# Performance work log

Measured on AMD Instinct MI355X. Metric: run time of the kernel, lower is better.

Reference implementation:

```python
import jax, jax.numpy as jnp
import numpy as np

B, S, E = 1, 2048, 4096
H, D = 32, 128  # num_heads, head_dim


def setup_inputs() -> dict:
    key = jax.random.key(0)
    k1, k2, k3 = jax.random.split(key, 3)
    hidden_states = jax.random.normal(k1, (B, S, E), dtype=jnp.float32)
    # real RoPE tables (half-rotation / llama-style), base 10000
    inv_freq = 1.0 / (10000.0 ** (np.arange(0, D, 2, dtype=np.float32) / D))  # [D/2]
    pos = np.arange(S, dtype=np.float32)
    freqs = np.outer(pos, inv_freq)                      # [S, D/2]
    emb = np.concatenate([freqs, freqs], axis=-1)        # [S, D]
    cos = jnp.asarray(np.cos(emb), dtype=jnp.float32)
    sin = jnp.asarray(np.sin(emb), dtype=jnp.float32)
    w_pack = jax.random.normal(k2, (3 * E, E), dtype=jnp.float32) * (E ** -0.5)
    w_o = jax.random.normal(k3, (E, E), dtype=jnp.float32) * (E ** -0.5)
    return {"hidden_states": hidden_states, "cos": cos, "sin": sin,
            "w_pack": w_pack, "w_o": w_o}


def _rotate_half(x):
    x1, x2 = jnp.split(x, 2, axis=-1)
    return jnp.concatenate([-x2, x1], axis=-1)


def reference(hidden_states, cos, sin, w_pack, w_o):
    # fused QKV projection (W_pack, no bias)
    qkv = jnp.einsum('bse,fe->bsf', hidden_states, w_pack)      # [B,S,3E]
    q, k, v = jnp.split(qkv, 3, axis=-1)
    q = q.reshape(B, S, H, D)
    k = k.reshape(B, S, H, D)
    v = v.reshape(B, S, H, D)
    # RoPE (7B path; is_13b=False)
    c = cos[None, :, None, :]
    s = sin[None, :, None, :]
    q = q * c + _rotate_half(q) * s
    k = k * c + _rotate_half(k) * s
    # causal attention (prefill, empty past KV cache)
    scale = 1.0 / jnp.sqrt(jnp.asarray(D, dtype=q.dtype))
    scores = jnp.einsum('bqhd,bkhd->bhqk', q, k) * scale        # [B,H,S,S]
    causal = jnp.tril(jnp.ones((S, S), dtype=bool))
    scores = jnp.where(causal[None, None], scores, jnp.asarray(-1e30, scores.dtype))
    probs = jax.nn.softmax(scores, axis=-1)
    attn = jnp.einsum('bhqk,bkhd->bqhd', probs, v)              # [B,S,H,D]
    attn = attn.reshape(B, S, H * D)
    # output projection
    return jnp.einsum('bsf,ef->bse', attn, w_o)
```

## Files before the change

kernel.cpp:

```cpp
#include <hip/hip_runtime.h>

typedef unsigned short u16;
typedef unsigned int   u32;
typedef __attribute__((ext_vector_type(8))) short short8;
typedef __attribute__((ext_vector_type(4))) float f32x4;

__device__ __forceinline__ float b2f(u16 u) {
  union { float f; u32 i; } v; v.i = ((u32)u) << 16; return v.f;
}
__device__ __forceinline__ u16 f2b(float f) {
  union { float f; u32 i; } v; v.f = f;
  u32 r = v.i + 0x7fffu + ((v.i >> 16) & 1u);
  return (u16)(r >> 16);
}

__device__ __forceinline__ void gload_lds16(const void* g, void* l) {
  __builtin_amdgcn_global_load_lds(
      (const __attribute__((address_space(1))) void*)g,
      (__attribute__((address_space(3))) void*)l, 16, 0, 0);
}

template <int N> __device__ __forceinline__ void wait_vmcnt() {
  if constexpr (N == 0)      asm volatile("s_waitcnt vmcnt(0)" ::: "memory");
  else if constexpr (N == 2) asm volatile("s_waitcnt vmcnt(2)" ::: "memory");
  else if constexpr (N == 3) asm volatile("s_waitcnt vmcnt(3)" ::: "memory");
  else if constexpr (N == 4) asm volatile("s_waitcnt vmcnt(4)" ::: "memory");
  else if constexpr (N == 6) asm volatile("s_waitcnt vmcnt(6)" ::: "memory");
  else static_assert(N < 0, "unsupported vmcnt literal");
}

__device__ __forceinline__ ushort4 cvt4(float4 v) {
  ushort4 o;
  o.x = f2b(v.x); o.y = f2b(v.y); o.z = f2b(v.z); o.w = f2b(v.w);
  return o;
}

__global__ __launch_bounds__(256) void cvt_hp(const float* __restrict__ hs,
                                              const float* __restrict__ wp,
                                              u16* __restrict__ h_bf,
                                              u16* __restrict__ wp_bf) {
  const long H4 = 2097152, W4 = 12582912;
  for (long i = (long)blockIdx.x * 256 + threadIdx.x; i < H4 + W4;
       i += (long)gridDim.x * 256) {
    if (i < H4)
      ((ushort4*)h_bf)[i] = cvt4(((const float4*)hs)[i]);
    else
      ((ushort4*)wp_bf)[i - H4] = cvt4(((const float4*)wp)[i - H4]);
  }
}

__global__ __launch_bounds__(256) void cvt_bf16(const float* __restrict__ in,
                                                u16* __restrict__ out, int n4) {
  for (long i = (long)blockIdx.x * 256 + threadIdx.x; i < n4; i += (long)gridDim.x * 256)
    ((ushort4*)out)[i] = cvt4(((const float4*)in)[i]);
}

__device__ __forceinline__ short8 frag_ld64(const u16* base, int rbase, int kk,
                                            int fr, int fq) {
  const int r = rbase + fr;
  return *(const short8*)(base + r * 64 + ((((kk << 2) + fq) ^ (r & 7)) << 3));
}

__global__ __launch_bounds__(512, 2) void gemm8p(const u16* __restrict__ A,
                                                 const u16* __restrict__ B,
                                                 u16* __restrict__ Cq,
                                                 u16* __restrict__ VT,
                                                 int M, int N, int K) {
  constexpr int AE = 16384;
  constexpr int BUFSZ = AE + 12288;
  __shared__ u16 lds[2 * BUFSZ];
  const int tid = threadIdx.x;
  const int wid = tid >> 6, lane = tid & 63;
  const int fr = lane & 15, fq = lane >> 4;
  const int mA = (wid >> 2) * 128;
  const int nB = (wid & 3) * 48;

  const int nty = M >> 8;
  const int qx = gridDim.x >> 3;
  const int wg = (blockIdx.x & 7) * qx + (blockIdx.x >> 3);
  const int by = wg % nty, bx = wg / nty;
  const long row0 = (long)by * 256, col0 = (long)bx * 192;

  const int rr8 = tid >> 3;
  const int jl = (tid & 7) ^ (rr8 & 7);
  const u16* gA = A + (row0 + rr8) * (long)K + jl * 8;
  const u16* gB = B + (col0 + rr8) * (long)K + jl * 8;

  f32x4 acc[8][3];
#pragma unroll
  for (int m = 0; m < 8; ++m)
#pragma unroll
    for (int n = 0; n < 3; ++n) acc[m][n] = f32x4{0.f, 0.f, 0.f, 0.f};

  const int NT = K >> 6;

  auto stageA = [&](int i, int t) {
    gload_lds16(gA + (long)(i * 64) * K + (long)t * 64,
                lds + (t & 1) * BUFSZ + (i * 512 + tid) * 8);
  };
  auto stageB = [&](int i, int t) {
    gload_lds16(gB + (long)(i * 64) * K + (long)t * 64,
                lds + (t & 1) * BUFSZ + AE + (i * 512 + tid) * 8);
  };

#pragma unroll
  for (int i = 0; i < 4; ++i) stageA(i, 0);
#pragma unroll
  for (int i = 0; i < 3; ++i) stageB(i, 0);
#pragma unroll
  for (int i = 0; i < 3; ++i) stageB(i, 1);
  wait_vmcnt<3>();
  __builtin_amdgcn_s_barrier();

  for (int t = 0; t < NT; ++t) {
    const u16* SA = lds + (t & 1) * BUFSZ;
    const u16* SB = SA + AE;
    short8 a0[4], a1[4], b0[3], b1[3];

#pragma unroll
    for (int m = 0; m < 4; ++m) a0[m] = frag_ld64(SA, mA + m * 16, 0, fr, fq);
#pragma unroll
    for (int n = 0; n < 3; ++n) b0[n] = frag_ld64(SB, nB + n * 16, 0, fr, fq);
#pragma unroll
    for (int n = 0; n < 3; ++n) b1[n] = frag_ld64(SB, nB + n * 16, 1, fr, fq);
    if (t + 1 < NT) { stageA(0, t + 1); stageA(1, t + 1); }
    __builtin_amdgcn_s_setprio(1);
#pragma unroll
    for (int m = 0; m < 4; ++m)
#pragma unroll
      for (int n = 0; n < 3; ++n)
        acc[m][n] = __builtin_amdgcn_mfma_f32_16x16x32_bf16(a0[m], b0[n], acc[m][n], 0, 0, 0);
    __builtin_amdgcn_s_setprio(0);
    asm volatile("s_waitcnt lgkmcnt(0)" ::: "memory");
    __builtin_amdgcn_s_barrier();

#pragma unroll
    for (int m = 0; m < 4; ++m) a1[m] = frag_ld64(SA, mA + 64 + m * 16, 0, fr, fq);
    if (t + 1 < NT) { stageA(2, t + 1); stageA(3, t + 1); }
    __builtin_amdgcn_s_setprio(1);
#pragma unroll
    for (int m = 0; m < 4; ++m)
#pragma unroll
      for (int n = 0; n < 3; ++n)
        acc[4 + m][n] = __builtin_amdgcn_mfma_f32_16x16x32_bf16(a1[m], b0[n], acc[4 + m][n], 0, 0, 0);
    __builtin_amdgcn_s_setprio(0);
    __builtin_amdgcn_s_barrier();

#pragma unroll
    for (int m = 0; m < 4; ++m) a0[m] = frag_ld64(SA, mA + m * 16, 1, fr, fq);
    if (t + 2 < NT) { stageB(0, t + 2); stageB(1, t + 2); }
    __builtin_amdgcn_s_setprio(1);
#pragma unroll
    for (int m = 0; m < 4; ++m)
#pragma unroll
      for (int n = 0; n < 3; ++n)
        acc[m][n] = __builtin_amdgcn_mfma_f32_16x16x32_bf16(a0[m], b1[n], acc[m][n], 0, 0, 0);
    __builtin_amdgcn_s_setprio(0);
    __builtin_amdgcn_s_barrier();

#pragma unroll
    for (int m = 0; m < 4; ++m) a1[m] = frag_ld64(SA, mA + 64 + m * 16, 1, fr, fq);
    if (t + 2 < NT) stageB(2, t + 2);
    __builtin_amdgcn_s_setprio(1);
#pragma unroll
    for (int m = 0; m < 4; ++m)
#pragma unroll
      for (int n = 0; n < 3; ++n)
        acc[4 + m][n] = __builtin_amdgcn_mfma_f32_16x16x32_bf16(a1[m], b1[n], acc[4 + m][n], 0, 0, 0);
    __builtin_amdgcn_s_setprio(0);
    if (t + 2 < NT) wait_vmcnt<3>();
    else            wait_vmcnt<0>();
    __builtin_amdgcn_s_barrier();
  }

#pragma unroll
  for (int m = 0; m < 8; ++m)
#pragma unroll
    for (int n = 0; n < 3; ++n) {
      const long c = col0 + nB + n * 16 + fr;
      const long rb = row0 + mA + m * 16 + fq * 4;
      if (c >= 8192) {
        ushort4 o;
        o.x = f2b(acc[m][n][0]); o.y = f2b(acc[m][n][1]);
        o.z = f2b(acc[m][n][2]); o.w = f2b(acc[m][n][3]);
        *(ushort4*)(VT + (c - 8192) * 2048 + rb) = o;
      } else {
#pragma unroll
        for (int j = 0; j < 4; ++j) Cq[(rb + j) * N + c] = f2b(acc[m][n][j]);
      }
    }
}

__global__ __launch_bounds__(256, 2) void gemm2_128(const u16* __restrict__ A,
                                                    const u16* __restrict__ B,
                                                    float* __restrict__ C,
                                                    int M, int N, int K) {
  constexpr int AE = 8192;
  constexpr int BUFSZ = 2 * AE;
  __shared__ u16 lds[2 * BUFSZ];
  const int tid = threadIdx.x;
  const int wid = tid >> 6, lane = tid & 63;
  const int fr = lane & 15, fq = lane >> 4;
  const int mA = (wid >> 1) * 64;
  const int nB = (wid & 1) * 64;

  const int nty = M >> 7;
  const int qx = gridDim.x >> 3;
  const int wg = (blockIdx.x & 7) * qx + (blockIdx.x >> 3);
  const int by = wg % nty, bx = wg / nty;
  const long row0 = (long)by * 128, col0 = (long)bx * 128;

  const int rr8 = tid >> 3;
  const int jl = (tid & 7) ^ (rr8 & 7);
  const u16* gA = A + (row0 + rr8) * (long)K + jl * 8;
  const u16* gB = B + (col0 + rr8) * (long)K + jl * 8;

  f32x4 acc[4][4];
#pragma unroll
  for (int m = 0; m < 4; ++m)
#pragma unroll
    for (int n = 0; n < 4; ++n) acc[m][n] = f32x4{0.f, 0.f, 0.f, 0.f};

  const int NT = K >> 6;

  auto stageA = [&](int i, int t) {
    gload_lds16(gA + (long)(i * 32) * K + (long)t * 64,
                lds + (t & 1) * BUFSZ + (i * 256 + tid) * 8);
  };
  auto stageB = [&](int i, int t) {
    gload_lds16(gB + (long)(i * 32) * K + (long)t * 64,
                lds + (t & 1) * BUFSZ + AE + (i * 256 + tid) * 8);
  };

#pragma unroll
  for (int i = 0; i < 4; ++i) stageA(i, 0);
#pragma unroll
  for (int i = 0; i < 4; ++i) stageB(i, 0);
#pragma unroll
  for (int i = 0; i < 4; ++i) stageB(i, 1);
  wait_vmcnt<4>();
  __builtin_amdgcn_s_barrier();

  for (int t = 0; t < NT; ++t) {
    const u16* SA = lds + (t & 1) * BUFSZ;
    const u16* SB = SA + AE;
    short8 a[2], b0[4], b1[4];

    a[0] = frag_ld64(SA, mA +  0, 0, fr, fq);
    a[1] = frag_ld64(SA, mA + 16, 0, fr, fq);
#pragma unroll
    for (int n = 0; n < 4; ++n) b0[n] = frag_ld64(SB, nB + n * 16, 0, fr, fq);
#pragma unroll
    for (int n = 0; n < 4; ++n) b1[n] = frag_ld64(SB, nB + n * 16, 1, fr, fq);
    if (t + 1 < NT) { stageA(0, t + 1); stageA(1, t + 1); }
    __builtin_amdgcn_s_setprio(1);
#pragma unroll
    for (int m = 0; m < 2; ++m)
#pragma unroll
      for (int n = 0; n < 4; ++n)
        acc[m][n] = __builtin_amdgcn_mfma_f32_16x16x32_bf16(a[m], b0[n], acc[m][n], 0, 0, 0);
    __builtin_amdgcn_s_setprio(0);
    asm volatile("s_waitcnt lgkmcnt(0)" ::: "memory");
    __builtin_amdgcn_s_barrier();

    a[0] = frag_ld64(SA, mA + 32, 0, fr, fq);
    a[1] = frag_ld64(SA, mA + 48, 0, fr, fq);
    if (t + 1 < NT) { stageA(2, t + 1); stageA(3, t + 1); }
    __builtin_amdgcn_s_setprio(1);
#pragma unroll
    for (int m = 0; m < 2; ++m)
#pragma unroll
      for (int n = 0; n < 4; ++n)
        acc[2 + m][n] = __builtin_amdgcn_mfma_f32_16x16x32_bf16(a[m], b0[n], acc[2 + m][n], 0, 0, 0);
    __builtin_amdgcn_s_setprio(0);
    __builtin_amdgcn_s_barrier();

    a[0] = frag_ld64(SA, mA +  0, 1, fr, fq);
    a[1] = frag_ld64(SA, mA + 16, 1, fr, fq);
    if (t + 2 < NT) { stageB(0, t + 2); stageB(1, t + 2); }
    __builtin_amdgcn_s_setprio(1);
#pragma unroll
    for (int m = 0; m < 2; ++m)
#pragma unroll
      for (int n = 0; n < 4; ++n)
        acc[m][n] = __builtin_amdgcn_mfma_f32_16x16x32_bf16(a[m], b1[n], acc[m][n], 0, 0, 0);
    __builtin_amdgcn_s_setprio(0);
    __builtin_amdgcn_s_barrier();

    a[0] = frag_ld64(SA, mA + 32, 1, fr, fq);
    a[1] = frag_ld64(SA, mA + 48, 1, fr, fq);
    if (t + 2 < NT) { stageB(2, t + 2); stageB(3, t + 2); }
    __builtin_amdgcn_s_setprio(1);
#pragma unroll
    for (int m = 0; m < 2; ++m)
#pragma unroll
      for (int n = 0; n < 4; ++n)
        acc[2 + m][n] = __builtin_amdgcn_mfma_f32_16x16x32_bf16(a[m], b1[n], acc[2 + m][n], 0, 0, 0);
    __builtin_amdgcn_s_setprio(0);
    if (t + 2 < NT) wait_vmcnt<4>();
    else            wait_vmcnt<0>();
    __builtin_amdgcn_s_barrier();
  }

#pragma unroll
  for (int m = 0; m < 4; ++m)
#pragma unroll
    for (int n = 0; n < 4; ++n)
#pragma unroll
      for (int j = 0; j < 4; ++j) {
        const long r = row0 + mA + m * 16 + fq * 4 + j;
        const long c = col0 + nB + n * 16 + fr;
        C[r * N + c] = acc[m][n][j];
      }
}

__global__ __launch_bounds__(256) void rope_qk(u16* __restrict__ qkv,
                                               const float* __restrict__ cosb,
                                               const float* __restrict__ sinb) {
  const int idx = blockIdx.x * 256 + threadIdx.x;
  const int dq  = idx & 15;
  const int h   = (idx >> 4) & 31;
  const int seg = (idx >> 9) & 1;
  const int s   = idx >> 10;
  const int d0  = dq * 4;
  u16* base = qkv + (long)s * 12288 + seg * 4096 + h * 128;
  const ushort4 x1 = *(const ushort4*)(base + d0);
  const ushort4 x2 = *(const ushort4*)(base + d0 + 64);
  const float4 c1 = *(const float4*)(cosb + s * 128 + d0);
  const float4 s1 = *(const float4*)(sinb + s * 128 + d0);
  const float4 c2 = *(const float4*)(cosb + s * 128 + d0 + 64);
  const float4 s2 = *(const float4*)(sinb + s * 128 + d0 + 64);
  const float scale = seg ? 1.0f : 0.08838834764831845f;
  float x1f[4] = {b2f(x1.x), b2f(x1.y), b2f(x1.z), b2f(x1.w)};
  float x2f[4] = {b2f(x2.x), b2f(x2.y), b2f(x2.z), b2f(x2.w)};
  const float c1a[4] = {c1.x, c1.y, c1.z, c1.w}, s1a[4] = {s1.x, s1.y, s1.z, s1.w};
  const float c2a[4] = {c2.x, c2.y, c2.z, c2.w}, s2a[4] = {s2.x, s2.y, s2.z, s2.w};
  ushort4 o1, o2;
  u16* o1p = (u16*)&o1; u16* o2p = (u16*)&o2;
#pragma unroll
  for (int j = 0; j < 4; ++j) {
    o1p[j] = f2b((x1f[j] * c1a[j] - x2f[j] * s1a[j]) * scale);
    o2p[j] = f2b((x2f[j] * c2a[j] + x1f[j] * s2a[j]) * scale);
  }
  *(ushort4*)(base + d0) = o1;
  *(ushort4*)(base + d0 + 64) = o2;
}

__global__ __launch_bounds__(256) void attn_fwd(const u16* __restrict__ Qb,
                                                const u16* __restrict__ Kb,
                                                const u16* __restrict__ Vt,
                                                u16* __restrict__ Ob) {
  const int h = blockIdx.y;
  const int tid = threadIdx.x;
  const int wid = tid >> 6, lane = tid & 63;
  const int fr = lane & 15, fq = lane >> 4;

  __shared__ u16 Ks[2][64 * 128];
  __shared__ u16 Vts[2][128 * 64];
  __shared__ u16 Ps[4][32 * 72];

  short8 ones;
#pragma unroll
  for (int i = 0; i < 8; ++i) ones[i] = (short)0x3F80;

  auto stage = [&](int t, int buf) {
    const int kv0 = t * 64;
#pragma unroll
    for (int i = 0; i < 4; ++i) {
      const int c = wid * 4 + i;
      {
        const int r = c * 4 + (lane >> 4);
        const int p = lane & 15;
        const int jsrc = p ^ (r & 7);
        gload_lds16(Kb + (long)(kv0 + r) * 12288 + h * 128 + jsrc * 8,
                    (char*)Ks[buf] + c * 1024);
      }
      {
        const int d = c * 8 + (lane >> 3);
        const int p = lane & 7;
        const int jsrc = p ^ (d & 7);
        gload_lds16(Vt + (long)(h * 128 + d) * 2048 + kv0 + jsrc * 8,
                    (char*)Vts[buf] + c * 1024);
      }
    }
  };

#pragma unroll
  for (int pass = 0; pass < 2; ++pass) {
    const int qt = pass == 0 ? (int)blockIdx.x : 15 - (int)blockIdx.x;
    const int q0 = qt * 128;
    const int nt = 2 * qt + 2;
    const int wq_hi = q0 + wid * 32 + 31;

    short8 qf[2][4];
#pragma unroll
    for (int m = 0; m < 2; ++m) {
      const long qrow = q0 + wid * 32 + m * 16 + fr;
#pragma unroll
      for (int kk = 0; kk < 4; ++kk)
        qf[m][kk] = *(const short8*)(Qb + qrow * 12288 + h * 128 + kk * 32 + fq * 8);
    }

    f32x4 Oacc[2][8], Sacc[2];
#pragma unroll
    for (int m = 0; m < 2; ++m) {
#pragma unroll
      for (int f = 0; f < 8; ++f) Oacc[m][f] = f32x4{0.f, 0.f, 0.f, 0.f};
      Sacc[m] = f32x4{0.f, 0.f, 0.f, 0.f};
    }
    float mrun[2];
    mrun[0] = -1e30f; mrun[1] = -1e30f;

    stage(0, 0);
    wait_vmcnt<0>();
    __builtin_amdgcn_s_barrier();

    for (int t = 0; t < nt; ++t) {
      const int cur = t & 1;
      const int kv0 = t * 64;
      if (t + 1 < nt) stage(t + 1, cur ^ 1);

      if (kv0 <= wq_hi) {
        f32x4 S[2][4];
#pragma unroll
        for (int m = 0; m < 2; ++m)
#pragma unroll
          for (int n = 0; n < 4; ++n) S[m][n] = f32x4{0.f, 0.f, 0.f, 0.f};
        __builtin_amdgcn_s_setprio(1);
#pragma unroll
        for (int kk = 0; kk < 4; ++kk) {
          short8 kf[4];
#pragma unroll
          for (int n = 0; n < 4; ++n) {
            const int r = n * 16 + fr;
            const int p = (kk * 4 + fq) ^ (r & 7);
            kf[n] = *(const short8*)((const char*)Ks[cur] + r * 256 + p * 16);
          }
#pragma unroll
          for (int m = 0; m < 2; ++m)
#pragma unroll
            for (int n = 0; n < 4; ++n)
              S[m][n] = __builtin_amdgcn_mfma_f32_16x16x32_bf16(kf[n], qf[m][kk], S[m][n], 0, 0, 0);
        }
        __builtin_amdgcn_s_setprio(0);

        float P[2][4][4];
        float alr[2][4];
#pragma unroll
        for (int m = 0; m < 2; ++m) {
          const int qi = q0 + wid * 32 + m * 16 + fr;
          float tm = -1e30f;
#pragma unroll
          for (int n = 0; n < 4; ++n)
#pragma unroll
            for (int j = 0; j < 4; ++j) {
              const int kv = kv0 + n * 16 + fq * 4 + j;
              const float s = (kv <= qi) ? S[m][n][j] : -1e30f;
              P[m][n][j] = s;
              tm = fmaxf(tm, s);
            }
          tm = fmaxf(tm, __shfl_xor(tm, 16));
          tm = fmaxf(tm, __shfl_xor(tm, 32));
          const float mn = fmaxf(mrun[m], tm);
          const float al = __expf(mrun[m] - mn);
          mrun[m] = mn;
#pragma unroll
          for (int n = 0; n < 4; ++n)
#pragma unroll
            for (int j = 0; j < 4; ++j)
              P[m][n][j] = __expf(P[m][n][j] - mn);
#pragma unroll
          for (int j = 0; j < 4; ++j) alr[m][j] = __shfl(al, fq * 4 + j);
#pragma unroll
          for (int f = 0; f < 8; ++f) {
            f32x4 o = Oacc[m][f];
#pragma unroll
            for (int j = 0; j < 4; ++j) o[j] *= alr[m][j];
            Oacc[m][f] = o;
          }
#pragma unroll
          for (int j = 0; j < 4; ++j) Sacc[m][j] *= alr[m][j];
        }

#pragma unroll
        for (int m = 0; m < 2; ++m)
#pragma unroll
          for (int n = 0; n < 4; ++n) {
            ushort4 w;
            u16* wp_ = (u16*)&w;
#pragma unroll
            for (int j = 0; j < 4; ++j) wp_[j] = f2b(P[m][n][j]);
            *(ushort4*)(Ps[wid] + (m * 16 + fr) * 72 + n * 16 + fq * 4) = w;
          }

        __builtin_amdgcn_s_setprio(1);
#pragma unroll
        for (int kb = 0; kb < 2; ++kb) {
          short8 pa0 = *(const short8*)(Ps[wid] + (fr) * 72 + kb * 32 + fq * 8);
          short8 pa1 = *(const short8*)(Ps[wid] + (16 + fr) * 72 + kb * 32 + fq * 8);
#pragma unroll
          for (int f = 0; f < 8; ++f) {
            const int d = f * 16 + fr;
            const int p = (kb * 4 + fq) ^ (d & 7);
            short8 vf = *(const short8*)((const char*)Vts[cur] + d * 128 + p * 16);
            Oacc[0][f] = __builtin_amdgcn_mfma_f32_16x16x32_bf16(pa0, vf, Oacc[0][f], 0, 0, 0);
            Oacc[1][f] = __builtin_amdgcn_mfma_f32_16x16x32_bf16(pa1, vf, Oacc[1][f], 0, 0, 0);
          }
          Sacc[0] = __builtin_amdgcn_mfma_f32_16x16x32_bf16(pa0, ones, Sacc[0], 0, 0, 0);
          Sacc[1] = __builtin_amdgcn_mfma_f32_16x16x32_bf16(pa1, ones, Sacc[1], 0, 0, 0);
        }
        __builtin_amdgcn_s_setprio(0);
      }
      wait_vmcnt<0>();
      __builtin_amdgcn_s_barrier();
    }

#pragma unroll
    for (int m = 0; m < 2; ++m)
#pragma unroll
      for (int j = 0; j < 4; ++j) {
        const float inv = 1.f / Sacc[m][j];
        const long r = q0 + wid * 32 + m * 16 + fq * 4 + j;
#pragma unroll
        for (int f = 0; f < 8; ++f)
          Ob[r * 4096 + h * 128 + f * 16 + fr] = f2b(Oacc[m][f][j] * inv);
      }
  }
}

extern "C" void kernel_launch(void* const* d_in, const int* in_sizes, int n_in,
                              void* d_out, int out_size, void* d_ws, size_t ws_size,
                              hipStream_t stream) {
  const float* hs   = (const float*)d_in[0];
  const float* cosb = (const float*)d_in[1];
  const float* sinb = (const float*)d_in[2];
  const float* wp   = (const float*)d_in[3];
  const float* wo   = (const float*)d_in[4];
  float* out = (float*)d_out;
  char* ws = (char*)d_ws;

  u16* h_bf  = (u16*)(ws);
  u16* attn  = (u16*)(ws);
  u16* wp_bf = (u16*)(ws + 16777216);
  u16* wo_bf = (u16*)(ws + 16777216);
  u16* qkv   = (u16*)(ws + 121634816);
  u16* vt    = (u16*)(ws + 171966464);

  cvt_hp<<<4096, 256, 0, stream>>>(hs, wp, h_bf, wp_bf);
  gemm8p<<<512, 512, 0, stream>>>(h_bf, wp_bf, qkv, vt, 2048, 12288, 4096);
  cvt_bf16<<<2048, 256, 0, stream>>>(wo, wo_bf, 4194304);
  rope_qk<<<8192, 256, 0, stream>>>(qkv, cosb, sinb);
  attn_fwd<<<dim3(8, 32), 256, 0, stream>>>(qkv, qkv + 4096, vt, attn);
  gemm2_128<<<512, 256, 0, stream>>>(attn, wo_bf, out, 2048, 4096, 4096);
}
```

Baseline: 434.1 us.

## Split attention into one block per q-tile, fuse wo conversion into rope

The attention kernel now launches one block per (head, q-tile) instead of each block handling two paired q-tiles in sequence, and sets launch bounds for two blocks per CU. K stays double-buffered, but V is single-buffered and loaded in the same iteration it is used, with an extra barrier. The running-max rescale is skipped unless the new max exceeds the old one by more than a threshold, and the P tile in LDS uses an XOR swizzle instead of padding. The wo fp32-to-bf16 conversion is merged into the RoPE launch to remove one kernel launch. Together these aim for more blocks in flight and less rescale work, at the cost of some load-latency exposure and extra synchronisation per tile.

```diff
diff --git a/kernel.cpp b/kernel.cpp
--- a/kernel.cpp
+++ b/kernel.cpp
@@ -47,12 +47,6 @@
     else
       ((ushort4*)wp_bf)[i - H4] = cvt4(((const float4*)wp)[i - H4]);
   }
-}
-
-__global__ __launch_bounds__(256) void cvt_bf16(const float* __restrict__ in,
-                                                u16* __restrict__ out, int n4) {
-  for (long i = (long)blockIdx.x * 256 + threadIdx.x; i < n4; i += (long)gridDim.x * 256)
-    ((ushort4*)out)[i] = cvt4(((const float4*)in)[i]);
 }
 
 __device__ __forceinline__ short8 frag_ld64(const u16* base, int rbase, int kk,
@@ -314,9 +308,18 @@
       }
 }
 
-__global__ __launch_bounds__(256) void rope_qk(u16* __restrict__ qkv,
+__global__ __launch_bounds__(256) void rope_wo(u16* __restrict__ qkv,
                                                const float* __restrict__ cosb,
-                                               const float* __restrict__ sinb) {
+                                               const float* __restrict__ sinb,
+                                               const float* __restrict__ wo,
+                                               u16* __restrict__ wo_bf) {
+  if (blockIdx.x >= 8192) {
+    const int n4 = 4194304;
+    for (long i = (long)(blockIdx.x - 8192) * 256 + threadIdx.x; i < n4;
+         i += (long)2048 * 256)
+      ((ushort4*)wo_bf)[i] = cvt4(((const float4*)wo)[i]);
+    return;
+  }
   const int idx = blockIdx.x * 256 + threadIdx.x;
   const int dq  = idx & 15;
   const int h   = (idx >> 4) & 31;
@@ -346,186 +349,201 @@
   *(ushort4*)(base + d0 + 64) = o2;
 }
 
-__global__ __launch_bounds__(256) void attn_fwd(const u16* __restrict__ Qb,
-                                                const u16* __restrict__ Kb,
-                                                const u16* __restrict__ Vt,
-                                                u16* __restrict__ Ob) {
-  const int h = blockIdx.y;
+__global__ __launch_bounds__(256, 2) void attn_fwd(const u16* __restrict__ Qb,
+                                                   const u16* __restrict__ Kb,
+                                                   const u16* __restrict__ Vt,
+                                                   u16* __restrict__ Ob) {
+  const int bid = blockIdx.x;
+  const int half = bid >> 8, ii = bid & 255;
+  const int h = (ii >> 4) | (half << 4);
+  const int qt = half ? 15 - (ii & 15) : (ii & 15);
+  const int q0 = qt * 128;
+  const int nt = 2 * qt + 2;
   const int tid = threadIdx.x;
   const int wid = tid >> 6, lane = tid & 63;
   const int fr = lane & 15, fq = lane >> 4;
 
   __shared__ u16 Ks[2][64 * 128];
-  __shared__ u16 Vts[2][128 * 64];
-  __shared__ u16 Ps[4][32 * 72];
+  __shared__ u16 Vts[128 * 64];
+  __shared__ u16 Ps[4][32 * 64];
 
   short8 ones;
 #pragma unroll
   for (int i = 0; i < 8; ++i) ones[i] = (short)0x3F80;
 
-  auto stage = [&](int t, int buf) {
+  auto stageK = [&](int t, int buf) {
     const int kv0 = t * 64;
 #pragma unroll
     for (int i = 0; i < 4; ++i) {
       const int c = wid * 4 + i;
-      {
-        const int r = c * 4 + (lane >> 4);
-        const int p = lane & 15;
-        const int jsrc = p ^ (r & 7);
-        gload_lds16(Kb + (long)(kv0 + r) * 12288 + h * 128 + jsrc * 8,
-                    (char*)Ks[buf] + c * 1024);
-      }
-      {
-        const int d = c * 8 + (lane >> 3);
-        const int p = lane & 7;
-        const int jsrc = p ^ (d & 7);
-        gload_lds16(Vt + (long)(h * 128 + d) * 2048 + kv0 + jsrc * 8,
-                    (char*)Vts[buf] + c * 1024);
-      }
+      const int r = c * 4 + (lane >> 4);
+      const int p = lane & 15;
+      const int jsrc = p ^ (r & 7);
+      gload_lds16(Kb + (long)(kv0 + r) * 12288 + h * 128 + jsrc * 8,
+                  (char*)Ks[buf] + c * 1024);
     }
   };
-
-#pragma unroll
-  for (int pass = 0; pass < 2; ++pass) {
-    const int qt = pass == 0 ? (int)blockIdx.x : 15 - (int)blockIdx.x;
-    const int q0 = qt * 128;
-    const int nt = 2 * qt + 2;
-    const int wq_hi = q0 + wid * 32 + 31;
-
-    short8 qf[2][4];
-#pragma unroll
-    for (int m = 0; m < 2; ++m) {
-      const long qrow = q0 + wid * 32 + m * 16 + fr;
-#pragma unroll
-      for (int kk = 0; kk < 4; ++kk)
-        qf[m][kk] = *(const short8*)(Qb + qrow * 12288 + h * 128 + kk * 32 + fq * 8);
+  auto stageV = [&](int t) {
+    const int kv0 = t * 64;
+#pragma unroll
+    for (int i = 0; i < 4; ++i) {
+      const int c = wid * 4 + i;
+      const int d = c * 8 + (lane >> 3);
+      const int p = lane & 7;
+      const int jsrc = p ^ (d & 7);
+      gload_lds16(Vt + (long)(h * 128 + d) * 2048 + kv0 + jsrc * 8,
+                  (char*)Vts + c * 1024);
     }
-
-    f32x4 Oacc[2][8], Sacc[2];
-#pragma unroll
-    for (int m = 0; m < 2; ++m) {
-#pragma unroll
-      for (int f = 0; f < 8; ++f) Oacc[m][f] = f32x4{0.f, 0.f, 0.f, 0.f};
-      Sacc[m] = f32x4{0.f, 0.f, 0.f, 0.f};
-    }
-    float mrun[2];
-    mrun[0] = -1e30f; mrun[1] = -1e30f;
-
-    stage(0, 0);
-    wait_vmcnt<0>();
-    __builtin_amdgcn_s_barrier();
-
-    for (int t = 0; t < nt; ++t) {
-      const int cur = t & 1;
-      const int kv0 = t * 64;
-      if (t + 1 < nt) stage(t + 1, cur ^ 1);
-
-      if (kv0 <= wq_hi) {
-        f32x4 S[2][4];
+  };
+
+  const int wq_hi = q0 + wid * 32 + 31;
+
+  short8 qf[2][4];
+#pragma unroll
+  for (int m = 0; m < 2; ++m) {
+    const long qrow = q0 + wid * 32 + m * 16 + fr;
+#pragma unroll
+    for (int kk = 0; kk < 4; ++kk)
+      qf[m][kk] = *(const short8*)(Qb + qrow * 12288 + h * 128 + kk * 32 + fq * 8);
+  }
+
+  f32x4 Oacc[2][8], Sacc[2];
+#pragma unroll
+  for (int m = 0; m < 2; ++m) {
+#pragma unroll
+    for (int f = 0; f < 8; ++f) Oacc[m][f] = f32x4{0.f, 0.f, 0.f, 0.f};
+    Sacc[m] = f32x4{0.f, 0.f, 0.f, 0.f};
+  }
+  float mrun[2];
+  mrun[0] = -1e30f; mrun[1] = -1e30f;
+
+  stageK(0, 0);
+  wait_vmcnt<0>();
+  __builtin_amdgcn_s_barrier();
+
+  for (int t = 0; t < nt; ++t) {
+    const int cur = t & 1;
+    const int kv0 = t * 64;
+    stageV(t);
+    if (t + 1 < nt) stageK(t + 1, cur ^ 1);
+
+    const bool skip = kv0 > wq_hi;
+    float P[2][4][4];
+    if (!skip) {
+      f32x4 S[2][4];
+#pragma unroll
+      for (int m = 0; m < 2; ++m)
+#pragma unroll
+        for (int n = 0; n < 4; ++n) S[m][n] = f32x4{0.f, 0.f, 0.f, 0.f};
+      __builtin_amdgcn_s_setprio(1);
+#pragma unroll
+      for (int kk = 0; kk < 4; ++kk) {
+        short8 kf[4];
+#pragma unroll
+        for (int n = 0; n < 4; ++n) {
+          const int r = n * 16 + fr;
+          const int p = (kk * 4 + fq) ^ (r & 7);
+          kf[n] = *(const short8*)((const char*)Ks[cur] + r * 256 + p * 16);
+        }
 #pragma unroll
         for (int m = 0; m < 2; ++m)
 #pragma unroll
-          for (int n = 0; n < 4; ++n) S[m][n] = f32x4{0.f, 0.f, 0.f, 0.f};
-        __builtin_amdgcn_s_setprio(1);
-#pragma unroll
-        for (int kk = 0; kk < 4; ++kk) {
-          short8 kf[4];
-#pragma unroll
-          for (int n = 0; n < 4; ++n) {
-            const int r = n * 16 + fr;
-            const int p = (kk * 4 + fq) ^ (r & 7);
-            kf[n] = *(const short8*)((const char*)Ks[cur] + r * 256 + p * 16);
+          for (int n = 0; n < 4; ++n)
+            S[m][n] = __builtin_amdgcn_mfma_f32_16x16x32_bf16(kf[n], qf[m][kk], S[m][n], 0, 0, 0);
+      }
+      __builtin_amdgcn_s_setprio(0);
+
+#pragma unroll
+      for (int m = 0; m < 2; ++m) {
+        const int qi = q0 + wid * 32 + m * 16 + fr;
+        float tm = -1e30f;
+#pragma unroll
+        for (int n = 0; n < 4; ++n)
+#pragma unroll
+          for (int j = 0; j < 4; ++j) {
+            const int kv = kv0 + n * 16 + fq * 4 + j;
+            const float s = (kv <= qi) ? S[m][n][j] : -1e30f;
+            P[m][n][j] = s;
+            tm = fmaxf(tm, s);
           }
-#pragma unroll
-          for (int m = 0; m < 2; ++m)
-#pragma unroll
-            for (int n = 0; n < 4; ++n)
-              S[m][n] = __builtin_amdgcn_mfma_f32_16x16x32_bf16(kf[n], qf[m][kk], S[m][n], 0, 0, 0);
-        }
-        __builtin_amdgcn_s_setprio(0);
-
-        float P[2][4][4];
-        float alr[2][4];
-#pragma unroll
-        for (int m = 0; m < 2; ++m) {
-          const int qi = q0 + wid * 32 + m * 16 + fr;
-          float tm = -1e30f;
-#pragma unroll
-          for (int n = 0; n < 4; ++n)
-#pragma unroll
-            for (int j = 0; j < 4; ++j) {
-              const int kv = kv0 + n * 16 + fq * 4 + j;
-              const float s = (kv <= qi) ? S[m][n][j] : -1e30f;
-              P[m][n][j] = s;
-              tm = fmaxf(tm, s);
-            }
-          tm = fmaxf(tm, __shfl_xor(tm, 16));
-          tm = fmaxf(tm, __shfl_xor(tm, 32));
+        tm = fmaxf(tm, __shfl_xor(tm, 16));
+        tm = fmaxf(tm, __shfl_xor(tm, 32));
+        if (__any(tm > mrun[m] + 8.f)) {
           const float mn = fmaxf(mrun[m], tm);
           const float al = __expf(mrun[m] - mn);
           mrun[m] = mn;
-#pragma unroll
-          for (int n = 0; n < 4; ++n)
-#pragma unroll
-            for (int j = 0; j < 4; ++j)
-              P[m][n][j] = __expf(P[m][n][j] - mn);
-#pragma unroll
-          for (int j = 0; j < 4; ++j) alr[m][j] = __shfl(al, fq * 4 + j);
+          float alr[4];
+#pragma unroll
+          for (int j = 0; j < 4; ++j) alr[j] = __shfl(al, fq * 4 + j);
 #pragma unroll
           for (int f = 0; f < 8; ++f) {
             f32x4 o = Oacc[m][f];
 #pragma unroll
-            for (int j = 0; j < 4; ++j) o[j] *= alr[m][j];
+            for (int j = 0; j < 4; ++j) o[j] *= alr[j];
             Oacc[m][f] = o;
           }
 #pragma unroll
-          for (int j = 0; j < 4; ++j) Sacc[m][j] *= alr[m][j];
+          for (int j = 0; j < 4; ++j) Sacc[m][j] *= alr[j];
         }
-
-#pragma unroll
-        for (int m = 0; m < 2; ++m)
-#pragma unroll
-          for (int n = 0; n < 4; ++n) {
-            ushort4 w;
-            u16* wp_ = (u16*)&w;
-#pragma unroll
-            for (int j = 0; j < 4; ++j) wp_[j] = f2b(P[m][n][j]);
-            *(ushort4*)(Ps[wid] + (m * 16 + fr) * 72 + n * 16 + fq * 4) = w;
-          }
-
-        __builtin_amdgcn_s_setprio(1);
-#pragma unroll
-        for (int kb = 0; kb < 2; ++kb) {
-          short8 pa0 = *(const short8*)(Ps[wid] + (fr) * 72 + kb * 32 + fq * 8);
-          short8 pa1 = *(const short8*)(Ps[wid] + (16 + fr) * 72 + kb * 32 + fq * 8);
-#pragma unroll
-          for (int f = 0; f < 8; ++f) {
-            const int d = f * 16 + fr;
-            const int p = (kb * 4 + fq) ^ (d & 7);
-            short8 vf = *(const short8*)((const char*)Vts[cur] + d * 128 + p * 16);
-            Oacc[0][f] = __builtin_amdgcn_mfma_f32_16x16x32_bf16(pa0, vf, Oacc[0][f], 0, 0, 0);
-            Oacc[1][f] = __builtin_amdgcn_mfma_f32_16x16x32_bf16(pa1, vf, Oacc[1][f], 0, 0, 0);
-          }
-          Sacc[0] = __builtin_amdgcn_mfma_f32_16x16x32_bf16(pa0, ones, Sacc[0], 0, 0, 0);
-          Sacc[1] = __builtin_amdgcn_mfma_f32_16x16x32_bf16(pa1, ones, Sacc[1], 0, 0, 0);
+#pragma unroll
+        for (int n = 0; n < 4; ++n)
+#pragma unroll
+          for (int j = 0; j < 4; ++j)
+            P[m][n][j] = __expf(P[m][n][j] - mrun[m]);
+      }
+
+#pragma unroll
+      for (int m = 0; m < 2; ++m)
+#pragma unroll
+        for (int n = 0; n < 4; ++n) {
+          ushort4 w;
+          u16* wp_ = (u16*)&w;
+#pragma unroll
+          for (int j = 0; j < 4; ++j) wp_[j] = f2b(P[m][n][j]);
+          const int off = (m * 16 + fr) * 128 + ((n * 32 + fq * 8) ^ ((fr & 7) << 4));
+          *(ushort4*)((char*)Ps[wid] + off) = w;
         }
-        __builtin_amdgcn_s_setprio(0);
+    }
+
+    if (t + 1 < nt) wait_vmcnt<4>();
+    else            wait_vmcnt<0>();
+    __builtin_amdgcn_s_barrier();
+
+    if (!skip) {
+      __builtin_amdgcn_s_setprio(1);
+#pragma unroll
+      for (int kb = 0; kb < 2; ++kb) {
+        const int o0 = (fr) * 128 + ((kb * 64 + fq * 16) ^ ((fr & 7) << 4));
+        const int o1 = (16 + fr) * 128 + ((kb * 64 + fq * 16) ^ ((fr & 7) << 4));
+        short8 pa0 = *(const short8*)((const char*)Ps[wid] + o0);
+        short8 pa1 = *(const short8*)((const char*)Ps[wid] + o1);
+#pragma unroll
+        for (int f = 0; f < 8; ++f) {
+          const int d = f * 16 + fr;
+          const int p = (kb * 4 + fq) ^ (d & 7);
+          short8 vf = *(const short8*)((const char*)Vts + d * 128 + p * 16);
+          Oacc[0][f] = __builtin_amdgcn_mfma_f32_16x16x32_bf16(pa0, vf, Oacc[0][f], 0, 0, 0);
+          Oacc[1][f] = __builtin_amdgcn_mfma_f32_16x16x32_bf16(pa1, vf, Oacc[1][f], 0, 0, 0);
+        }
+        Sacc[0] = __builtin_amdgcn_mfma_f32_16x16x32_bf16(pa0, ones, Sacc[0], 0, 0, 0);
+        Sacc[1] = __builtin_amdgcn_mfma_f32_16x16x32_bf16(pa1, ones, Sacc[1], 0, 0, 0);
       }
-      wait_vmcnt<0>();
-      __builtin_amdgcn_s_barrier();
+      __builtin_amdgcn_s_setprio(0);
     }
-
-#pragma unroll
-    for (int m = 0; m < 2; ++m)
-#pragma unroll
-      for (int j = 0; j < 4; ++j) {
-        const float inv = 1.f / Sacc[m][j];
-        const long r = q0 + wid * 32 + m * 16 + fq * 4 + j;
-#pragma unroll
-        for (int f = 0; f < 8; ++f)
-          Ob[r * 4096 + h * 128 + f * 16 + fr] = f2b(Oacc[m][f][j] * inv);
-      }
-  }
+    wait_vmcnt<0>();
+    __builtin_amdgcn_s_barrier();
+  }
+
+#pragma unroll
+  for (int m = 0; m < 2; ++m)
+#pragma unroll
+    for (int j = 0; j < 4; ++j) {
+      const float inv = 1.f / Sacc[m][j];
+      const long r = q0 + wid * 32 + m * 16 + fq * 4 + j;
+#pragma unroll
+      for (int f = 0; f < 8; ++f)
+        Ob[r * 4096 + h * 128 + f * 16 + fr] = f2b(Oacc[m][f][j] * inv);
+    }
 }
 
 extern "C" void kernel_launch(void* const* d_in, const int* in_sizes, int n_in,
@@ -548,8 +566,7 @@
 
   cvt_hp<<<4096, 256, 0, stream>>>(hs, wp, h_bf, wp_bf);
   gemm8p<<<512, 512, 0, stream>>>(h_bf, wp_bf, qkv, vt, 2048, 12288, 4096);
-  cvt_bf16<<<2048, 256, 0, stream>>>(wo, wo_bf, 4194304);
-  rope_qk<<<8192, 256, 0, stream>>>(qkv, cosb, sinb);
-  attn_fwd<<<dim3(8, 32), 256, 0, stream>>>(qkv, qkv + 4096, vt, attn);
+  rope_wo<<<10240, 256, 0, stream>>>(qkv, cosb, sinb, wo, wo_bf);
+  attn_fwd<<<512, 256, 0, stream>>>(qkv, qkv + 4096, vt, attn);
   gemm2_128<<<512, 256, 0, stream>>>(attn, wo_bf, out, 2048, 4096, 4096);
 }
```

Result: faster. 423.4 us (-2.5%).
